# Kernel optimization log

Hardware: AMD Instinct MI355X
Metric: run time of the kernel (lower is better)

Reference implementation:

```python
import jax, jax.numpy as jnp
import numpy as np

D_MODEL = 768
NUM_HEAD = 12
D_K = D_MODEL // NUM_HEAD
NEG_BIG = -1e9


def setup_inputs() -> dict:
    key = jax.random.key(0)
    ks = jax.random.split(key, 16)
    B, S, D = 16, 512, D_MODEL
    scale = 1.0 / np.sqrt(D)
    inp = {
        "q": jax.random.normal(ks[0], (B, S, D), jnp.float32),
        "k": jax.random.normal(ks[1], (B, S, D), jnp.float32),
        "v": jax.random.normal(ks[2], (B, S, D), jnp.float32),
        # padding mask: 1 where masked, broadcast over heads and query dim
        "mask": jax.random.randint(ks[3], (B, 1, 1, S), 0, 2).astype(jnp.float32),
        # adjacency bias broadcast over heads
        "adj": jax.random.uniform(ks[4], (B, 1, S, S), jnp.float32),
        "Wq": jax.random.normal(ks[5], (D, D), jnp.float32) * scale,
        "bq": jnp.zeros((D,), jnp.float32),
        "Wk": jax.random.normal(ks[6], (D, D), jnp.float32) * scale,
        "bk": jnp.zeros((D,), jnp.float32),
        "Wv": jax.random.normal(ks[7], (D, D), jnp.float32) * scale,
        "bv": jnp.zeros((D,), jnp.float32),
        "Wo": jax.random.normal(ks[8], (D, D), jnp.float32) * scale,
        "bo": jnp.zeros((D,), jnp.float32),
    }
    return inp


def reference(q, k, v, mask, adj, Wq, bq, Wk, bk, Wv, bv, Wo, bo):
    B, S, D = q.shape
    H, dk = NUM_HEAD, D_K

    def proj(x, W, b):
        # nn.Linear: x @ W.T + b, then split heads -> [B, H, S, dk]
        y = jnp.einsum('bsd,ed->bse', x, W) + b
        return y.reshape(B, S, H, dk).transpose(0, 2, 1, 3)

    qh = proj(q, Wq, bq)
    kh = proj(k, Wk, bk)
    vh = proj(v, Wv, bv)

    scores = jnp.einsum('bhqd,bhkd->bhqk', qh, kh) / jnp.sqrt(jnp.float32(dk))
    scores = scores + mask * NEG_BIG + adj  # broadcast over heads
    attn = jax.nn.softmax(scores, axis=-1)
    x = jnp.einsum('bhqk,bhkd->bhqd', attn, vh)
    x = x.transpose(0, 2, 1, 3).reshape(B, S, D)
    return jnp.einsum('bsd,ed->bse', x, Wo) + bo
```

## Files before the change

kernel.cpp:

```cpp
#include <hip/hip_runtime.h>
#include <hip/hip_bf16.h>

#define SEQ 512
#define DM 768
#define NH 12
#define DK 64
#define NB 16
#define WN (DM * DM)
#define HE ((size_t)NB * SEQ * DM)
#define BSS ((size_t)NB * SEQ * SEQ)

typedef __attribute__((ext_vector_type(8))) _Float16 f16x8;
typedef __attribute__((ext_vector_type(4))) float f32x4;

static __device__ __forceinline__ void gload16(const void* g, void* lds) {
    __builtin_amdgcn_global_load_lds(
        (const __attribute__((address_space(1))) unsigned int*)g,
        (__attribute__((address_space(3))) unsigned int*)lds, 16, 0, 0);
}

__global__ __launch_bounds__(256) void convert_wa(
    const float* __restrict__ Wq, const float* __restrict__ Wk,
    const float* __restrict__ Wv, const float* __restrict__ Wo,
    const float* __restrict__ adj, const float* __restrict__ mask,
    _Float16* __restrict__ dst, _Float16* __restrict__ adjm)
{
    const size_t W4 = 4u * WN;
    size_t i8 = ((size_t)blockIdx.x * 256 + threadIdx.x) * 8;
    f16x8 h;
    if (i8 < W4) {
        unsigned int s = (unsigned int)(i8 / WN);
        const float* src = s == 0 ? Wq : s == 1 ? Wk : s == 2 ? Wv : Wo;
        size_t off = i8 - (size_t)s * WN;
        float4 a = *(const float4*)(src + off);
        float4 b = *(const float4*)(src + off + 4);
        h[0] = (_Float16)a.x; h[1] = (_Float16)a.y; h[2] = (_Float16)a.z; h[3] = (_Float16)a.w;
        h[4] = (_Float16)b.x; h[5] = (_Float16)b.y; h[6] = (_Float16)b.z; h[7] = (_Float16)b.w;
        *(f16x8*)(dst + i8) = h;
    } else {
        size_t j = i8 - W4;
        int b = (int)(j >> 18);
        int col = (int)(j & (SEQ - 1));
        float4 a0 = *(const float4*)(adj + j);
        float4 a1 = *(const float4*)(adj + j + 4);
        const float* mp = mask + ((size_t)b << 9) + col;
        float4 m0 = *(const float4*)(mp);
        float4 m1 = *(const float4*)(mp + 4);
        h[0] = (_Float16)(a0.x - 30000.0f * m0.x);
        h[1] = (_Float16)(a0.y - 30000.0f * m0.y);
        h[2] = (_Float16)(a0.z - 30000.0f * m0.z);
        h[3] = (_Float16)(a0.w - 30000.0f * m0.w);
        h[4] = (_Float16)(a1.x - 30000.0f * m1.x);
        h[5] = (_Float16)(a1.y - 30000.0f * m1.y);
        h[6] = (_Float16)(a1.z - 30000.0f * m1.z);
        h[7] = (_Float16)(a1.w - 30000.0f * m1.w);
        *(f16x8*)(adjm + j) = h;
    }
}

__global__ __launch_bounds__(256) void proj_qkv(
    const float* __restrict__ Aq, const float* __restrict__ Ak,
    const float* __restrict__ Av, const _Float16* __restrict__ Wh,
    const float* __restrict__ bq, const float* __restrict__ bk, const float* __restrict__ bv,
    _Float16* __restrict__ P1, _Float16* __restrict__ P2, _Float16* __restrict__ P3)
{
    __shared__ float As[128][32];
    __shared__ _Float16 Bs[128][32];
    const int f = blockIdx.x;
    const int lg = (f & 7) * 144 + (f >> 3);
    const int sel = lg / 384;
    const int rem = lg - sel * 384;
    const int bm = (rem / 6) * 128, bn = (rem % 6) * 128;
    const float* A = sel == 0 ? Aq : sel == 1 ? Ak : Av;
    const _Float16* W = Wh + (size_t)sel * WN;
    const float* bias = sel == 0 ? bq : sel == 1 ? bk : bv;
    _Float16* O = sel == 0 ? P1 : sel == 1 ? P2 : P3;

    const int t = threadIdx.x, lane = t & 63, w = t >> 6;
    const int wm = w >> 1, wn = w & 1, g = lane >> 4, r16 = lane & 15;
    const int lrow = lane >> 2, lcol = (lane & 3) * 8;
    const int arow = lane >> 3, acol = ((lane & 7) ^ (lane >> 3)) * 4;

    f32x4 acc[4][4] = {};

    const float*    ga  = A + (size_t)(bm + w * 32 + arow) * DM + acol;
    const _Float16* gb0 = W + (size_t)(bn + w * 32 + lrow) * DM + lcol;
    const _Float16* gb1 = gb0 + (size_t)16 * DM;
    const int s0 = ((2 * g)     ^ (r16 & 7)) * 4;
    const int s1 = ((2 * g + 1) ^ (r16 & 7)) * 4;

    for (int kk = 0; kk < DM; kk += 32) {
        gload16(ga + kk,              &As[w * 32][0]);
        gload16(ga + 8  * DM + kk,    &As[w * 32 + 8][0]);
        gload16(ga + 16 * DM + kk,    &As[w * 32 + 16][0]);
        gload16(ga + 24 * DM + kk,    &As[w * 32 + 24][0]);
        gload16(gb0 + kk, &Bs[w * 32][0]);
        gload16(gb1 + kk, &Bs[w * 32 + 16][0]);
        __syncthreads();
        f16x8 af[4], bf[4];
        #pragma unroll
        for (int mi = 0; mi < 4; ++mi) {
            const int row = wm * 64 + mi * 16 + r16;
            f32x4 x0 = *(f32x4*)&As[row][s0];
            f32x4 x1 = *(f32x4*)&As[row][s1];
            f16x8 h;
            h[0] = (_Float16)x0[0]; h[1] = (_Float16)x0[1];
            h[2] = (_Float16)x0[2]; h[3] = (_Float16)x0[3];
            h[4] = (_Float16)x1[0]; h[5] = (_Float16)x1[1];
            h[6] = (_Float16)x1[2]; h[7] = (_Float16)x1[3];
            af[mi] = h;
        }
        #pragma unroll
        for (int ni = 0; ni < 4; ++ni)
            bf[ni] = *(f16x8*)&Bs[wn * 64 + ni * 16 + r16][g * 8];
        #pragma unroll
        for (int mi = 0; mi < 4; ++mi)
            #pragma unroll
            for (int ni = 0; ni < 4; ++ni)
                acc[mi][ni] = __builtin_amdgcn_mfma_f32_16x16x32_f16(af[mi], bf[ni], acc[mi][ni], 0, 0, 0);
        __syncthreads();
    }
    #pragma unroll
    for (int ni = 0; ni < 4; ++ni) {
        int n = bn + wn * 64 + ni * 16 + r16;
        float bv_ = bias[n];
        #pragma unroll
        for (int mi = 0; mi < 4; ++mi) {
            #pragma unroll
            for (int r = 0; r < 4; ++r) {
                int m = bm + wm * 64 + mi * 16 + g * 4 + r;
                O[(size_t)m * DM + n] = (_Float16)(acc[mi][ni][r] + bv_);
            }
        }
    }
}

__global__ __launch_bounds__(256) void proj_o(
    const _Float16* __restrict__ A, const _Float16* __restrict__ W,
    const float* __restrict__ bias, float* __restrict__ O32)
{
    __shared__ _Float16 As[128][32];
    __shared__ _Float16 Bs[128][32];
    const int f = blockIdx.x;
    const int lg = (f & 7) * 48 + (f >> 3);
    const int bm = (lg / 6) * 128, bn = (lg % 6) * 128;
    const int t = threadIdx.x, lane = t & 63, w = t >> 6;
    const int wm = w >> 1, wn = w & 1, g = lane >> 4, r16 = lane & 15;
    const int lrow = lane >> 2, lcol = (lane & 3) * 8;

    f32x4 acc[4][4] = {};

    const _Float16* ga0 = A + (size_t)(bm + w * 32 + lrow) * DM + lcol;
    const _Float16* ga1 = ga0 + (size_t)16 * DM;
    const _Float16* gb0 = W + (size_t)(bn + w * 32 + lrow) * DM + lcol;
    const _Float16* gb1 = gb0 + (size_t)16 * DM;

    for (int kk = 0; kk < DM; kk += 32) {
        gload16(ga0 + kk, &As[w * 32][0]);
        gload16(ga1 + kk, &As[w * 32 + 16][0]);
        gload16(gb0 + kk, &Bs[w * 32][0]);
        gload16(gb1 + kk, &Bs[w * 32 + 16][0]);
        __syncthreads();
        f16x8 af[4], bf[4];
        #pragma unroll
        for (int mi = 0; mi < 4; ++mi)
            af[mi] = *(f16x8*)&As[wm * 64 + mi * 16 + r16][g * 8];
        #pragma unroll
        for (int ni = 0; ni < 4; ++ni)
            bf[ni] = *(f16x8*)&Bs[wn * 64 + ni * 16 + r16][g * 8];
        #pragma unroll
        for (int mi = 0; mi < 4; ++mi)
            #pragma unroll
            for (int ni = 0; ni < 4; ++ni)
                acc[mi][ni] = __builtin_amdgcn_mfma_f32_16x16x32_f16(af[mi], bf[ni], acc[mi][ni], 0, 0, 0);
        __syncthreads();
    }
    #pragma unroll
    for (int ni = 0; ni < 4; ++ni) {
        int n = bn + wn * 64 + ni * 16 + r16;
        float bv_ = bias[n];
        #pragma unroll
        for (int mi = 0; mi < 4; ++mi) {
            #pragma unroll
            for (int r = 0; r < 4; ++r) {
                int m = bm + wm * 64 + mi * 16 + g * 4 + r;
                O32[(size_t)m * DM + n] = acc[mi][ni][r] + bv_;
            }
        }
    }
}

#define VSWI(d, kcol) ((d) * 72 + ((((kcol) * 2) ^ ((((d) >> 3) & 7) << 4)) >> 1))
__global__ __launch_bounds__(256) void attn(
    const _Float16* __restrict__ Qp, const _Float16* __restrict__ Kp,
    const _Float16* __restrict__ Vp, const _Float16* __restrict__ Adjm,
    _Float16* __restrict__ X)
{
    __shared__ _Float16 Ks[2][64 * 64];
    __shared__ _Float16 Vt[2][64 * 72];
    __shared__ _Float16 Ps[4][16][72];
    const int id = blockIdx.x;
    const int lid = (id & 7) * 192 + (id >> 3);
    const int h = lid % NH, qb = (lid / NH) & 7, b = lid / (NH * 8);
    const int t = threadIdx.x, lane = t & 63, w = t >> 6;
    const int g = lane >> 4, r16 = lane & 15;
    const int srow = t >> 2, sc = (t & 3) * 16;

    const _Float16* Qg = Qp + (size_t)(b * SEQ + qb * 64 + w * 16 + r16) * DM + h * DK;
    const f16x8 qf0 = *(const f16x8*)(Qg + g * 8);
    const f16x8 qf1 = *(const f16x8*)(Qg + 32 + g * 8);

    const _Float16* Kbh   = Kp + (size_t)(b * SEQ) * DM + h * DK;
    const _Float16* Vbase = Vp + (size_t)(b * SEQ) * DM + h * DK + sc;
    const _Float16* Abase = Adjm + ((size_t)b << 18)
                                 + (size_t)(qb * 64 + w * 16 + g * 4) * SEQ + r16;

    uint4 vv[2];
    _Float16 am[16];

#define STAGEK(KB, BUF) { _Pragma("unroll") for (int j_ = 0; j_ < 2; ++j_) { \
        const _Float16* src_ = Kbh + (size_t)((KB) * 64 + w * 16 + j_ * 8 + (lane >> 3)) * DM \
                              + (((lane & 7) ^ (lane >> 3)) * 8); \
        gload16(src_, &Ks[BUF][(w * 16 + j_ * 8) * 64]); } }
#define LOADV(KB) { const _Float16* vp_ = Vbase + (size_t)((KB) * 64 + srow) * DM; \
        vv[0] = ((const uint4*)vp_)[0]; vv[1] = ((const uint4*)vp_)[1]; }
#define LOADA(KB) { _Pragma("unroll") for (int r = 0; r < 4; ++r) \
        _Pragma("unroll") for (int cb = 0; cb < 4; ++cb) \
            am[r * 4 + cb] = Abase[(size_t)r * SEQ + (KB) * 64 + cb * 16]; }

    STAGEK(0, 0);
    __builtin_amdgcn_sched_barrier(0);
    LOADV(0);
    LOADA(0);

    float l_lane[4] = {0.f, 0.f, 0.f, 0.f};
    f32x4 o[4] = {};

    #pragma unroll
    for (int kb = 0; kb < 8; ++kb) {
        const int buf = kb & 1;
        {
            union { uint4 u[2]; _Float16 hh[16]; } cv;
            cv.u[0] = vv[0]; cv.u[1] = vv[1];
            _Float16* vt = &Vt[buf][0];
            #pragma unroll
            for (int i = 0; i < 16; ++i) vt[VSWI(sc + i, srow)] = cv.hh[i];
        }
        asm volatile("s_waitcnt lgkmcnt(0)" ::: "memory");
        __builtin_amdgcn_sched_barrier(0);
        __builtin_amdgcn_s_barrier();
        __builtin_amdgcn_sched_barrier(0);

        f32x4 sf[4] = {};
        __builtin_amdgcn_s_setprio(1);
        #pragma unroll
        for (int cb = 0; cb < 4; ++cb) {
            const int R = cb * 16 + r16;
            f16x8 k0 = *(f16x8*)&Ks[buf][R * 64 + ((g ^ (r16 & 7)) * 8)];
            f16x8 k1 = *(f16x8*)&Ks[buf][R * 64 + (((4 + g) ^ (r16 & 7)) * 8)];
            sf[cb] = __builtin_amdgcn_mfma_f32_16x16x32_f16(qf0, k0, sf[cb], 0, 0, 0);
            sf[cb] = __builtin_amdgcn_mfma_f32_16x16x32_f16(qf1, k1, sf[cb], 0, 0, 0);
        }
        __builtin_amdgcn_s_setprio(0);
        if (kb < 7) {
            STAGEK(kb + 1, buf ^ 1);
            __builtin_amdgcn_sched_barrier(0);
            LOADV(kb + 1);
        }
        #pragma unroll
        for (int cb = 0; cb < 4; ++cb)
            #pragma unroll
            for (int r = 0; r < 4; ++r) {
                float e = exp2f(fmaf(sf[cb][r], 0.18033688f,
                            fmaf((float)am[r * 4 + cb], 1.44269504f, -11.54156036f)));
                sf[cb][r] = e;
                l_lane[r] += e;
            }
        if (kb < 7) LOADA(kb + 1);
        #pragma unroll
        for (int cb = 0; cb < 4; ++cb)
            #pragma unroll
            for (int r = 0; r < 4; ++r)
                Ps[w][g * 4 + r][cb * 16 + r16] = (_Float16)sf[cb][r];
        __builtin_amdgcn_s_setprio(1);
        #pragma unroll
        for (int ks = 0; ks < 2; ++ks) {
            f16x8 pf = *(f16x8*)&Ps[w][r16][ks * 32 + g * 8];
            #pragma unroll
            for (int db = 0; db < 4; ++db) {
                f16x8 vf = *(f16x8*)&Vt[buf][VSWI(db * 16 + r16, ks * 32 + g * 8)];
                o[db] = __builtin_amdgcn_mfma_f32_16x16x32_f16(pf, vf, o[db], 0, 0, 0);
            }
        }
        __builtin_amdgcn_s_setprio(0);
    }
#undef STAGEK
#undef LOADV
#undef LOADA
    #pragma unroll
    for (int d = 1; d < 16; d <<= 1)
        #pragma unroll
        for (int r = 0; r < 4; ++r)
            l_lane[r] += __shfl_xor(l_lane[r], d);
    const int qrow = qb * 64 + w * 16 + g * 4;
    #pragma unroll
    for (int r = 0; r < 4; ++r) {
        float inv = 1.f / l_lane[r];
        _Float16* xp = X + (size_t)(b * SEQ + qrow + r) * DM + h * DK;
        #pragma unroll
        for (int db = 0; db < 4; ++db)
            xp[db * 16 + r16] = (_Float16)(o[db][r] * inv);
    }
}

extern "C" void kernel_launch(void* const* d_in, const int* in_sizes, int n_in,
                              void* d_out, int out_size, void* d_ws, size_t ws_size,
                              hipStream_t stream)
{
    const float* q    = (const float*)d_in[0];
    const float* k    = (const float*)d_in[1];
    const float* v    = (const float*)d_in[2];
    const float* mask = (const float*)d_in[3];
    const float* adj  = (const float*)d_in[4];
    const float* Wq   = (const float*)d_in[5];
    const float* bq   = (const float*)d_in[6];
    const float* Wk   = (const float*)d_in[7];
    const float* bk   = (const float*)d_in[8];
    const float* Wv   = (const float*)d_in[9];
    const float* bv   = (const float*)d_in[10];
    const float* Wo   = (const float*)d_in[11];
    const float* bo   = (const float*)d_in[12];
    float* out = (float*)d_out;

    _Float16* Wh = (_Float16*)d_ws;
    _Float16* P1 = Wh + 4 * WN;
    _Float16* P2 = P1 + HE;
    _Float16* P3 = P2 + HE;
    _Float16* AD = P3 + HE;
    _Float16* X  = AD + BSS;

    convert_wa<<<dim3(3200), dim3(256), 0, stream>>>(Wq, Wk, Wv, Wo, adj, mask, Wh, AD);
    proj_qkv<<<dim3(1152), dim3(256), 0, stream>>>(q, k, v, Wh, bq, bk, bv, P1, P2, P3);
    attn<<<dim3(1536), dim3(256), 0, stream>>>(P1, P2, P3, AD, X);
    proj_o<<<dim3(384), dim3(256), 0, stream>>>(X, Wh + 3 * WN, bo, out);
}
```

Measured before the change: 122.6 us.

## Triple-buffer LDS in QKV projection to overlap global loads with MFMA

```diff
diff --git a/kernel.cpp b/kernel.cpp
--- a/kernel.cpp
+++ b/kernel.cpp
@@ -64,8 +64,8 @@
     const float* __restrict__ bq, const float* __restrict__ bk, const float* __restrict__ bv,
     _Float16* __restrict__ P1, _Float16* __restrict__ P2, _Float16* __restrict__ P3)
 {
-    __shared__ float As[128][32];
-    __shared__ _Float16 Bs[128][32];
+    __shared__ float As[3][128][32];
+    __shared__ _Float16 Bs[3][128][32];
     const int f = blockIdx.x;
     const int lg = (f & 7) * 144 + (f >> 3);
     const int sel = lg / 384;
@@ -89,37 +89,51 @@
     const int s0 = ((2 * g)     ^ (r16 & 7)) * 4;
     const int s1 = ((2 * g + 1) ^ (r16 & 7)) * 4;
 
-    for (int kk = 0; kk < DM; kk += 32) {
-        gload16(ga + kk,              &As[w * 32][0]);
-        gload16(ga + 8  * DM + kk,    &As[w * 32 + 8][0]);
-        gload16(ga + 16 * DM + kk,    &As[w * 32 + 16][0]);
-        gload16(ga + 24 * DM + kk,    &As[w * 32 + 24][0]);
-        gload16(gb0 + kk, &Bs[w * 32][0]);
-        gload16(gb1 + kk, &Bs[w * 32 + 16][0]);
-        __syncthreads();
-        f16x8 af[4], bf[4];
-        #pragma unroll
-        for (int mi = 0; mi < 4; ++mi) {
-            const int row = wm * 64 + mi * 16 + r16;
-            f32x4 x0 = *(f32x4*)&As[row][s0];
-            f32x4 x1 = *(f32x4*)&As[row][s1];
-            f16x8 h;
-            h[0] = (_Float16)x0[0]; h[1] = (_Float16)x0[1];
-            h[2] = (_Float16)x0[2]; h[3] = (_Float16)x0[3];
-            h[4] = (_Float16)x1[0]; h[5] = (_Float16)x1[1];
-            h[6] = (_Float16)x1[2]; h[7] = (_Float16)x1[3];
-            af[mi] = h;
-        }
-        #pragma unroll
-        for (int ni = 0; ni < 4; ++ni)
-            bf[ni] = *(f16x8*)&Bs[wn * 64 + ni * 16 + r16][g * 8];
-        #pragma unroll
-        for (int mi = 0; mi < 4; ++mi)
-            #pragma unroll
-            for (int ni = 0; ni < 4; ++ni)
-                acc[mi][ni] = __builtin_amdgcn_mfma_f32_16x16x32_f16(af[mi], bf[ni], acc[mi][ni], 0, 0, 0);
-        __syncthreads();
-    }
+#define STAGE(KK, BUF) { \
+        gload16(ga + (KK),            &As[BUF][w * 32][0]); \
+        gload16(ga + 8  * DM + (KK),  &As[BUF][w * 32 + 8][0]); \
+        gload16(ga + 16 * DM + (KK),  &As[BUF][w * 32 + 16][0]); \
+        gload16(ga + 24 * DM + (KK),  &As[BUF][w * 32 + 24][0]); \
+        gload16(gb0 + (KK),           &Bs[BUF][w * 32][0]); \
+        gload16(gb1 + (KK),           &Bs[BUF][w * 32 + 16][0]); }
+#define VW6 asm volatile("s_waitcnt vmcnt(6)" ::: "memory");
+#define VW0 asm volatile("s_waitcnt vmcnt(0)" ::: "memory");
+#define BAR { __builtin_amdgcn_sched_barrier(0); __builtin_amdgcn_s_barrier(); \
+              __builtin_amdgcn_sched_barrier(0); }
+#define COMPUTE(BUF) { f16x8 af[4], bf[4]; \
+        _Pragma("unroll") for (int mi = 0; mi < 4; ++mi) { \
+            const int row = wm * 64 + mi * 16 + r16; \
+            f32x4 x0 = *(f32x4*)&As[BUF][row][s0]; \
+            f32x4 x1 = *(f32x4*)&As[BUF][row][s1]; \
+            f16x8 hh; \
+            hh[0] = (_Float16)x0[0]; hh[1] = (_Float16)x0[1]; \
+            hh[2] = (_Float16)x0[2]; hh[3] = (_Float16)x0[3]; \
+            hh[4] = (_Float16)x1[0]; hh[5] = (_Float16)x1[1]; \
+            hh[6] = (_Float16)x1[2]; hh[7] = (_Float16)x1[3]; \
+            af[mi] = hh; } \
+        _Pragma("unroll") for (int ni = 0; ni < 4; ++ni) \
+            bf[ni] = *(f16x8*)&Bs[BUF][wn * 64 + ni * 16 + r16][g * 8]; \
+        _Pragma("unroll") for (int mi = 0; mi < 4; ++mi) \
+            _Pragma("unroll") for (int ni = 0; ni < 4; ++ni) \
+                acc[mi][ni] = __builtin_amdgcn_mfma_f32_16x16x32_f16(af[mi], bf[ni], acc[mi][ni], 0, 0, 0); }
+
+    STAGE(0, 0);
+    #pragma unroll 1
+    for (int tt = 0; tt < 21; tt += 3) {
+        STAGE((tt + 1) * 32, 1); VW6; BAR; COMPUTE(0);
+        STAGE((tt + 2) * 32, 2); VW6; BAR; COMPUTE(1);
+        STAGE((tt + 3) * 32, 0); VW6; BAR; COMPUTE(2);
+    }
+    STAGE(22 * 32, 1); VW6; BAR; COMPUTE(0);
+    STAGE(23 * 32, 2); VW6; BAR; COMPUTE(1);
+    VW0; BAR; COMPUTE(2);
+
+#undef STAGE
+#undef VW6
+#undef VW0
+#undef BAR
+#undef COMPUTE
+
     #pragma unroll
     for (int ni = 0; ni < 4; ++ni) {
         int n = bn + wn * 64 + ni * 16 + r16;
```

New measurement: 124.1 us. No clear change (+1.2%).
